# Performance work log

Measured on AMD Instinct MI355X. Metric: run time of the kernel, lower is better.

Reference implementation:

```python
import jax, jax.numpy as jnp
import numpy as np

B, T_ENC, ENC, DEC, MEL = 32, 1024, 1024, 1024, 80


def setup_inputs() -> dict:
    key = jax.random.key(0)
    ks = jax.random.split(key, 10)
    s = lambda k, shape, sc=1.0: (jax.random.normal(k, shape, dtype=jnp.float32) * sc)
    return {
        "prev_mel_frame": s(ks[0], (B, MEL)),
        "encoder_outputs": s(ks[1], (B, T_ENC, ENC)),
        "h": s(ks[2], (B, DEC)),
        "c": s(ks[3], (B, DEC)),
        # AdditiveAttention learned scale vector (use_scale=True default)
        "attn_scale": s(ks[4], (ENC,), 0.05),
        # LSTMCell params: input dim = MEL + ENC, gates order i, f, c, o (Keras)
        "kernel": s(ks[5], (MEL + ENC, 4 * DEC), 0.02),
        "rec_kernel": s(ks[6], (DEC, 4 * DEC), 0.02),
        "bias": s(ks[7], (4 * DEC,), 0.02),
        # Dense projection to mel
        "proj_w": s(ks[8], (DEC, MEL), 0.02),
        "proj_b": s(ks[9], (MEL,), 0.02),
    }


def reference(prev_mel_frame, encoder_outputs, h, c,
              attn_scale, kernel, rec_kernel, bias, proj_w, proj_b):
    # Additive (Bahdanau) attention: scores[b,t] = sum_d scale_d * tanh(h[b,d] + enc[b,t,d])
    feat = jnp.tanh(h[:, None, :] + encoder_outputs)          # [B, T, D]
    scores = jnp.einsum("btd,d->bt", feat, attn_scale)         # [B, T]
    attn = jax.nn.softmax(scores, axis=-1)
    context = jnp.einsum("bt,btd->bd", attn, encoder_outputs)  # [B, ENC]

    # LSTMCell step on concat([prev_mel, context])
    x = jnp.concatenate([prev_mel_frame, context], axis=-1)    # [B, MEL+ENC]
    z = x @ kernel + h @ rec_kernel + bias                     # [B, 4*DEC]
    i, f, g, o = jnp.split(z, 4, axis=-1)
    i = jax.nn.sigmoid(i)
    f = jax.nn.sigmoid(f)
    o = jax.nn.sigmoid(o)
    c_new = f * c + i * jnp.tanh(g)
    h_new = o * jnp.tanh(c_new)

    mel_frame = h_new @ proj_w + proj_b                        # [B, MEL]
    return mel_frame, h_new, c_new
```

## Files before the change

### kernel.cpp

```cpp
#include <hip/hip_runtime.h>

#define BB 32
#define TT 1024
#define ENCD 1024
#define DECD 1024
#define MELD 80
#define KTOT (MELD + ENCD + DECD)
#define NZ (4 * DECD)
#define KCH 64
#define KC 34

__device__ float g_scores[BB * TT];
__device__ float g_cp[8 * BB * ENCD];
__device__ float g_ctx[BB * ENCD];
__device__ float g_zp[KC * BB * NZ];
__device__ float g_hn[BB * DECD];

__device__ __forceinline__ float tanh_fast(float x) {
    return 1.f - __fdividef(2.f, __expf(2.f * x) + 1.f);
}
__device__ __forceinline__ float sigmoid_fast(float x) {
    return __fdividef(1.f, 1.f + __expf(-x));
}

__global__ __launch_bounds__(256) void k_scores(const float* __restrict__ enc,
                                                const float* __restrict__ h,
                                                const float* __restrict__ scale) {
    int w = blockIdx.x * 4 + (threadIdx.x >> 6);
    int lane = threadIdx.x & 63;
    int b = w >> 10;
    const float4* ep = (const float4*)(enc + (size_t)w * ENCD);
    const float4* hp = (const float4*)(h + (size_t)b * DECD);
    const float4* sp = (const float4*)scale;
    float sum = 0.f;
#pragma unroll
    for (int j = 0; j < 4; j++) {
        int i = lane + j * 64;
        float4 e = ep[i], hv = hp[i], s = sp[i];
        sum += s.x * tanh_fast(hv.x + e.x);
        sum += s.y * tanh_fast(hv.y + e.y);
        sum += s.z * tanh_fast(hv.z + e.z);
        sum += s.w * tanh_fast(hv.w + e.w);
    }
#pragma unroll
    for (int off = 32; off > 0; off >>= 1) sum += __shfl_down(sum, off, 64);
    if (lane == 0) g_scores[w] = sum;
}

__global__ __launch_bounds__(256) void k_context(const float* __restrict__ enc) {
    int b = blockIdx.x, tt = blockIdx.y, tid = threadIdx.x;
    __shared__ float red[4];
    __shared__ float la[128];
    float v[4];
#pragma unroll
    for (int i = 0; i < 4; i++) v[i] = g_scores[b * TT + tid + i * 256];
    float m = fmaxf(fmaxf(v[0], v[1]), fmaxf(v[2], v[3]));
#pragma unroll
    for (int off = 32; off > 0; off >>= 1) m = fmaxf(m, __shfl_down(m, off, 64));
    if ((tid & 63) == 0) red[tid >> 6] = m;
    __syncthreads();
    m = fmaxf(fmaxf(red[0], red[1]), fmaxf(red[2], red[3]));
    __syncthreads();
    float s = 0.f;
#pragma unroll
    for (int i = 0; i < 4; i++) s += __expf(v[i] - m);
#pragma unroll
    for (int off = 32; off > 0; off >>= 1) s += __shfl_down(s, off, 64);
    if ((tid & 63) == 0) red[tid >> 6] = s;
    __syncthreads();
    s = red[0] + red[1] + red[2] + red[3];
    float inv = __fdividef(1.f, s);
    if (tid < 128) la[tid] = __expf(g_scores[b * TT + tt * 128 + tid] - m) * inv;
    __syncthreads();

    const float4* ep = (const float4*)(enc + ((size_t)b * TT + tt * 128) * ENCD) + tid;
    float ax = 0.f, ay = 0.f, az = 0.f, aw = 0.f;
#pragma unroll 8
    for (int t = 0; t < 128; t++) {
        float4 e = ep[(size_t)t * (ENCD / 4)];
        float w = la[t];
        ax = fmaf(w, e.x, ax); ay = fmaf(w, e.y, ay);
        az = fmaf(w, e.z, az); aw = fmaf(w, e.w, aw);
    }
    float4 r; r.x = ax; r.y = ay; r.z = az; r.w = aw;
    ((float4*)g_cp)[((size_t)tt * BB + b) * (ENCD / 4) + tid] = r;
}

__global__ __launch_bounds__(256) void k_ctxsum() {
    int i = blockIdx.x * 256 + threadIdx.x;
    float a = 0.f;
#pragma unroll
    for (int tt = 0; tt < 8; tt++) a += g_cp[tt * (BB * ENCD) + i];
    g_ctx[i] = a;
}

__global__ __launch_bounds__(256) void k_zmm(const float* __restrict__ pm,
                                             const float* __restrict__ h,
                                             const float* __restrict__ kern,
                                             const float* __restrict__ reck) {
    __shared__ float xs[KCH * 32];
    int jt = blockIdx.x & 15, kc = blockIdx.x >> 4;
    int k0 = kc * KCH;
    int kcount = min(KCH, KTOT - k0);
    int tid = threadIdx.x;
    for (int idx = tid; idx < kcount * 32; idx += 256) {
        int kk = idx >> 5, b = idx & 31;
        int k = k0 + kk;
        float v;
        if (k < MELD)             v = pm[b * MELD + k];
        else if (k < MELD + ENCD) v = g_ctx[b * ENCD + (k - MELD)];
        else                      v = h[b * DECD + (k - MELD - ENCD)];
        xs[idx] = v;
    }
    __syncthreads();
    int j = jt * 256 + tid;
    float acc[32];
#pragma unroll
    for (int b = 0; b < 32; b++) acc[b] = 0.f;
    for (int kk0 = 0; kk0 < kcount; kk0 += 8) {
        float w[8];
#pragma unroll
        for (int i = 0; i < 8; i++) {
            int k = k0 + kk0 + i;
            w[i] = (k < MELD + ENCD) ? kern[(size_t)k * NZ + j]
                                     : reck[(size_t)(k - MELD - ENCD) * NZ + j];
        }
#pragma unroll
        for (int i = 0; i < 8; i++) {
            const float* xr = xs + (kk0 + i) * 32;
#pragma unroll
            for (int b = 0; b < 32; b++) acc[b] = fmaf(xr[b], w[i], acc[b]);
        }
    }
#pragma unroll
    for (int b = 0; b < 32; b++) g_zp[((size_t)kc * BB + b) * NZ + j] = acc[b];
}

__global__ __launch_bounds__(256) void k_gates(const float* __restrict__ bias,
                                               const float* __restrict__ c,
                                               float* __restrict__ out) {
    int b = blockIdx.x >> 2, jq = blockIdx.x & 3;
    int j = jq * 256 + threadIdx.x;
    float zi = bias[j], zf = bias[1024 + j], zg = bias[2048 + j], zo = bias[3072 + j];
#pragma unroll 4
    for (int kc = 0; kc < KC; kc++) {
        const float* zp = g_zp + ((size_t)kc * BB + b) * NZ;
        zi += zp[j];
        zf += zp[1024 + j];
        zg += zp[2048 + j];
        zo += zp[3072 + j];
    }
    int idx = b * 1024 + j;
    float cn = sigmoid_fast(zf) * c[idx] + sigmoid_fast(zi) * tanh_fast(zg);
    float hn = sigmoid_fast(zo) * tanh_fast(cn);
    g_hn[idx] = hn;
    out[2560 + idx] = hn;
    out[35328 + idx] = cn;
}

__global__ __launch_bounds__(256) void k_proj(const float* __restrict__ pw,
                                              const float* __restrict__ pb,
                                              float* __restrict__ out) {
    __shared__ float lh[1024];
    __shared__ float pacc[2][MELD];
    int b = blockIdx.x, tid = threadIdx.x;
    for (int i = tid; i < 1024; i += 256) lh[i] = g_hn[b * 1024 + i];
    __syncthreads();
    int m = tid & 127;
    int g = tid >> 7;
    if (m < MELD) {
        float acc = 0.f;
        int d0 = g * 512;
#pragma unroll 8
        for (int d = d0; d < d0 + 512; d++) acc = fmaf(lh[d], pw[d * MELD + m], acc);
        pacc[g][m] = acc;
    }
    __syncthreads();
    if (tid < MELD) out[b * MELD + tid] = pacc[0][tid] + pacc[1][tid] + pb[tid];
}

extern "C" void kernel_launch(void* const* d_in, const int* in_sizes, int n_in,
                              void* d_out, int out_size, void* d_ws, size_t ws_size,
                              hipStream_t stream) {
    const float* pm   = (const float*)d_in[0];
    const float* enc  = (const float*)d_in[1];
    const float* h    = (const float*)d_in[2];
    const float* c    = (const float*)d_in[3];
    const float* asc  = (const float*)d_in[4];
    const float* kern = (const float*)d_in[5];
    const float* reck = (const float*)d_in[6];
    const float* bias = (const float*)d_in[7];
    const float* pw   = (const float*)d_in[8];
    const float* pb   = (const float*)d_in[9];
    float* out = (float*)d_out;

    k_scores <<<8192, 256, 0, stream>>>(enc, h, asc);
    k_context<<<dim3(32, 8), 256, 0, stream>>>(enc);
    k_ctxsum <<<128, 256, 0, stream>>>();
    k_zmm    <<<544, 256, 0, stream>>>(pm, h, kern, reck);
    k_gates  <<<128, 256, 0, stream>>>(bias, c, out);
    k_proj   <<<32, 256, 0, stream>>>(pw, pb, out);
}
```

Measured before the change: 300.8 us.

## Fuse attention scores, softmax and context into single-pass online-softmax kernel

Replaces the separate score, context and context-sum kernels with one kernel that reads each encoder row once, computes its score, and folds it into a running online-softmax context accumulator per wavefront, followed by a small combine kernel that merges 128 partials per batch. The goal is to avoid reading the 128 MB encoder tensor twice. In exchange it writes and rereads a 16 MB partial-context buffer and uses only 1024 blocks, each wavefront handling 8 rows serially.

```diff
diff --git a/kernel.cpp b/kernel.cpp
--- a/kernel.cpp
+++ b/kernel.cpp
@@ -9,9 +9,11 @@
 #define NZ (4 * DECD)
 #define KCH 64
 #define KC 34
-
-__device__ float g_scores[BB * TT];
-__device__ float g_cp[8 * BB * ENCD];
+#define NP 128
+
+__device__ float g_pctx[BB * NP * ENCD];
+__device__ float g_pm[BB * NP];
+__device__ float g_ps[BB * NP];
 __device__ float g_ctx[BB * ENCD];
 __device__ float g_zp[KC * BB * NZ];
 __device__ float g_hn[BB * DECD];
@@ -23,75 +25,77 @@
     return __fdividef(1.f, 1.f + __expf(-x));
 }
 
-__global__ __launch_bounds__(256) void k_scores(const float* __restrict__ enc,
-                                                const float* __restrict__ h,
-                                                const float* __restrict__ scale) {
-    int w = blockIdx.x * 4 + (threadIdx.x >> 6);
-    int lane = threadIdx.x & 63;
-    int b = w >> 10;
-    const float4* ep = (const float4*)(enc + (size_t)w * ENCD);
+__global__ __launch_bounds__(256) void k_attn(const float* __restrict__ enc,
+                                              const float* __restrict__ h,
+                                              const float* __restrict__ scale) {
+    int b = blockIdx.x, tt = blockIdx.y;
+    int tid = threadIdx.x, w = tid >> 6, lane = tid & 63;
     const float4* hp = (const float4*)(h + (size_t)b * DECD);
     const float4* sp = (const float4*)scale;
-    float sum = 0.f;
-#pragma unroll
-    for (int j = 0; j < 4; j++) {
-        int i = lane + j * 64;
-        float4 e = ep[i], hv = hp[i], s = sp[i];
-        sum += s.x * tanh_fast(hv.x + e.x);
-        sum += s.y * tanh_fast(hv.y + e.y);
-        sum += s.z * tanh_fast(hv.z + e.z);
-        sum += s.w * tanh_fast(hv.w + e.w);
-    }
-#pragma unroll
-    for (int off = 32; off > 0; off >>= 1) sum += __shfl_down(sum, off, 64);
-    if (lane == 0) g_scores[w] = sum;
-}
-
-__global__ __launch_bounds__(256) void k_context(const float* __restrict__ enc) {
-    int b = blockIdx.x, tt = blockIdx.y, tid = threadIdx.x;
-    __shared__ float red[4];
-    __shared__ float la[128];
-    float v[4];
-#pragma unroll
-    for (int i = 0; i < 4; i++) v[i] = g_scores[b * TT + tid + i * 256];
-    float m = fmaxf(fmaxf(v[0], v[1]), fmaxf(v[2], v[3]));
-#pragma unroll
-    for (int off = 32; off > 0; off >>= 1) m = fmaxf(m, __shfl_down(m, off, 64));
-    if ((tid & 63) == 0) red[tid >> 6] = m;
-    __syncthreads();
-    m = fmaxf(fmaxf(red[0], red[1]), fmaxf(red[2], red[3]));
-    __syncthreads();
-    float s = 0.f;
-#pragma unroll
-    for (int i = 0; i < 4; i++) s += __expf(v[i] - m);
-#pragma unroll
-    for (int off = 32; off > 0; off >>= 1) s += __shfl_down(s, off, 64);
-    if ((tid & 63) == 0) red[tid >> 6] = s;
-    __syncthreads();
-    s = red[0] + red[1] + red[2] + red[3];
-    float inv = __fdividef(1.f, s);
-    if (tid < 128) la[tid] = __expf(g_scores[b * TT + tt * 128 + tid] - m) * inv;
-    __syncthreads();
-
-    const float4* ep = (const float4*)(enc + ((size_t)b * TT + tt * 128) * ENCD) + tid;
-    float ax = 0.f, ay = 0.f, az = 0.f, aw = 0.f;
+    float4 hv[4], sv[4];
+#pragma unroll
+    for (int j = 0; j < 4; j++) { hv[j] = hp[lane + j * 64]; sv[j] = sp[lane + j * 64]; }
+
+    float m = -1e30f, s = 0.f;
+    float4 cx[4];
+#pragma unroll
+    for (int j = 0; j < 4; j++) { cx[j].x = cx[j].y = cx[j].z = cx[j].w = 0.f; }
+
+    int t0 = tt * 32 + w * 8;
+    for (int r = 0; r < 8; r++) {
+        const float4* rp = (const float4*)(enc + ((size_t)b * TT + t0 + r) * ENCD);
+        float4 e[4];
+#pragma unroll
+        for (int j = 0; j < 4; j++) e[j] = rp[lane + j * 64];
+        float p = 0.f;
+#pragma unroll
+        for (int j = 0; j < 4; j++) {
+            p += sv[j].x * tanh_fast(hv[j].x + e[j].x);
+            p += sv[j].y * tanh_fast(hv[j].y + e[j].y);
+            p += sv[j].z * tanh_fast(hv[j].z + e[j].z);
+            p += sv[j].w * tanh_fast(hv[j].w + e[j].w);
+        }
+#pragma unroll
+        for (int off = 1; off < 64; off <<= 1) p += __shfl_xor(p, off, 64);
+        float mn = fmaxf(m, p);
+        float al = __expf(m - mn);
+        float wt = __expf(p - mn);
+        s = s * al + wt;
+#pragma unroll
+        for (int j = 0; j < 4; j++) {
+            cx[j].x = cx[j].x * al + wt * e[j].x;
+            cx[j].y = cx[j].y * al + wt * e[j].y;
+            cx[j].z = cx[j].z * al + wt * e[j].z;
+            cx[j].w = cx[j].w * al + wt * e[j].w;
+        }
+        m = mn;
+    }
+    int pidx = (b * 32 + tt) * 4 + w;
+    float4* pc = (float4*)g_pctx + (size_t)pidx * (ENCD / 4);
+#pragma unroll
+    for (int j = 0; j < 4; j++) pc[lane + j * 64] = cx[j];
+    if (lane == 0) { g_pm[pidx] = m; g_ps[pidx] = s; }
+}
+
+__global__ __launch_bounds__(256) void k_combine() {
+    int b = blockIdx.x, dq = blockIdx.y, tid = threadIdx.x;
+    __shared__ float lm[NP], ls[NP], em[NP];
+    if (tid < NP) { lm[tid] = g_pm[b * NP + tid]; ls[tid] = g_ps[b * NP + tid]; }
+    __syncthreads();
+    float mg = -1e30f;
 #pragma unroll 8
-    for (int t = 0; t < 128; t++) {
-        float4 e = ep[(size_t)t * (ENCD / 4)];
-        float w = la[t];
-        ax = fmaf(w, e.x, ax); ay = fmaf(w, e.y, ay);
-        az = fmaf(w, e.z, az); aw = fmaf(w, e.w, aw);
-    }
-    float4 r; r.x = ax; r.y = ay; r.z = az; r.w = aw;
-    ((float4*)g_cp)[((size_t)tt * BB + b) * (ENCD / 4) + tid] = r;
-}
-
-__global__ __launch_bounds__(256) void k_ctxsum() {
-    int i = blockIdx.x * 256 + threadIdx.x;
-    float a = 0.f;
-#pragma unroll
-    for (int tt = 0; tt < 8; tt++) a += g_cp[tt * (BB * ENCD) + i];
-    g_ctx[i] = a;
+    for (int p = 0; p < NP; p++) mg = fmaxf(mg, lm[p]);
+    float sg = 0.f;
+#pragma unroll 8
+    for (int p = 0; p < NP; p++) sg += ls[p] * __expf(lm[p] - mg);
+    if (tid < NP) em[tid] = __expf(lm[tid] - mg);
+    __syncthreads();
+    int d = dq * 256 + tid;
+    float acc = 0.f;
+#pragma unroll 4
+    for (int p = 0; p < NP; p++)
+        acc = fmaf(g_pctx[((size_t)(b * NP + p)) * ENCD + d], em[p], acc);
+    g_ctx[b * ENCD + d] = __fdividef(acc, sg);
 }
 
 __global__ __launch_bounds__(256) void k_zmm(const float* __restrict__ pm,
@@ -194,9 +198,8 @@
     const float* pb   = (const float*)d_in[9];
     float* out = (float*)d_out;
 
-    k_scores <<<8192, 256, 0, stream>>>(enc, h, asc);
-    k_context<<<dim3(32, 8), 256, 0, stream>>>(enc);
-    k_ctxsum <<<128, 256, 0, stream>>>();
+    k_attn   <<<dim3(32, 32), 256, 0, stream>>>(enc, h, asc);
+    k_combine<<<dim3(32, 4), 256, 0, stream>>>();
     k_zmm    <<<544, 256, 0, stream>>>(pm, h, kern, reck);
     k_gates  <<<128, 256, 0, stream>>>(bias, c, out);
     k_proj   <<<32, 256, 0, stream>>>(pw, pb, out);
```

Result: slower. 315.7 us (+5.0%).
